# Kernel tuning notes

Hardware: AMD Instinct MI355X
Metric: run time of the kernel (lower is better)

## Reference

```python
import jax, jax.numpy as jnp
import numpy as np


def gcn_conv(x, src, dst, W, b, num_nodes):
    # PyG GCNConv: add self-loops, symmetric deg^-1/2 normalization, scatter-add.
    h = x @ W                                    # [N, out]
    loops = jnp.arange(num_nodes, dtype=src.dtype)
    s = jnp.concatenate([src, loops])            # [E+N]
    d = jnp.concatenate([dst, loops])            # [E+N]
    deg = jax.ops.segment_sum(jnp.ones_like(d, dtype=h.dtype), d, num_segments=num_nodes)
    dinv = jnp.where(deg > 0, jax.lax.rsqrt(deg), 0.0)
    norm = dinv[s] * dinv[d]                     # [E+N]
    msgs = h[s] * norm[:, None]                  # gather + scale  [E+N, out]
    out = jax.ops.segment_sum(msgs, d, num_segments=num_nodes)
    return out + b


NUM_GRAPHS = 512


def setup_inputs() -> dict:
    key = jax.random.key(0)
    ks = jax.random.split(key, 12)
    N, E, F = 50000, 400000, 128
    x = jax.random.normal(ks[0], (N, F), dtype=jnp.float32)
    edge_index = jax.random.randint(ks[1], (2, E), 0, N, dtype=jnp.int64)
    batch = jnp.sort(jax.random.randint(ks[2], (N,), 0, NUM_GRAPHS, dtype=jnp.int64))
    def lin(k, fi, fo):
        return jax.random.normal(k, (fi, fo), dtype=jnp.float32) * (1.0 / np.sqrt(fi))
    return {
        "x": x, "edge_index": edge_index, "batch": batch,
        "W1": lin(ks[3], F, 512), "b1": jnp.zeros((512,), jnp.float32),
        "W2": lin(ks[4], 512, 256), "b2": jnp.zeros((256,), jnp.float32),
        "W3": lin(ks[5], 256, 128), "b3": jnp.zeros((128,), jnp.float32),
        "W4": lin(ks[6], 128, 32), "b4": jnp.zeros((32,), jnp.float32),
        "W5": lin(ks[7], 32, 10), "b5": jnp.zeros((10,), jnp.float32),
    }


def reference(x, edge_index, batch, W1, b1, W2, b2, W3, b3, W4, b4, W5, b5):
    N = x.shape[0]
    src, dst = edge_index[0], edge_index[1]
    h = gcn_conv(x, src, dst, W1, b1, N)
    h = jax.nn.leaky_relu(h, negative_slope=0.01)
    h = gcn_conv(h, src, dst, W2, b2, N)          # [N, 256]
    embs = jax.ops.segment_max(h, batch, num_segments=NUM_GRAPHS)  # [G, 256]
    z = ((h @ W3 + b3) @ W4 + b4) @ W5 + b5       # [N, 10]
    out = jax.ops.segment_max(z, batch, num_segments=NUM_GRAPHS)   # [G, 10]
    return (out, embs)
```

## Files before the change

### kernel.cpp

```cpp
#include <hip/hip_runtime.h>
#include <math.h>

#define DIV_UP(a,b) (((a)+(b)-1)/(b))

typedef __attribute__((ext_vector_type(8))) short bf16x8;
typedef __attribute__((ext_vector_type(4))) float f32x4;

__device__ inline unsigned short f2b(float x) {
    unsigned int u = __float_as_uint(x);
    u += 0x7fffu + ((u >> 16) & 1u);
    return (unsigned short)(u >> 16);
}

__device__ inline void cvt8(uint4 v, float* a) {
    a[0] = __uint_as_float(v.x << 16); a[1] = __uint_as_float(v.x & 0xffff0000u);
    a[2] = __uint_as_float(v.y << 16); a[3] = __uint_as_float(v.y & 0xffff0000u);
    a[4] = __uint_as_float(v.z << 16); a[5] = __uint_as_float(v.z & 0xffff0000u);
    a[6] = __uint_as_float(v.w << 16); a[7] = __uint_as_float(v.w & 0xffff0000u);
}

__device__ inline void atomicMaxF(float* addr, float v) {
    if (v >= 0.f) atomicMax((int*)addr, __float_as_int(v));
    else          atomicMin((unsigned int*)addr, __float_as_uint(v));
}

__device__ inline void gl16(void* lds, const void* g) {
    __builtin_amdgcn_global_load_lds(
        (const __attribute__((address_space(1))) void*)g,
        (__attribute__((address_space(3))) void*)lds, 16, 0, 0);
}

__global__ void k_zero_i(int* p, int n) {
    int i = blockIdx.x * blockDim.x + threadIdx.x;
    if (i < n) p[i] = 0;
}

__global__ void k_hist(const int* __restrict__ dst, int* __restrict__ hist, int E) {
    int i = blockIdx.x * blockDim.x + threadIdx.x;
    if (i < E) atomicAdd(&hist[dst[i]], 1);
}

__global__ __launch_bounds__(256) void k_scan_bsum(const int* __restrict__ hist,
                                                   int* __restrict__ bsum, int N) {
    __shared__ int red[256];
    int t = threadIdx.x;
    int base = blockIdx.x * 1024 + t * 4;
    int s = 0;
    if (base + 3 < N) {
        int4 v = *(const int4*)&hist[base];
        s = v.x + v.y + v.z + v.w;
    } else {
        for (int j = 0; j < 4; ++j) if (base + j < N) s += hist[base + j];
    }
    red[t] = s;
    __syncthreads();
    for (int off = 128; off >= 1; off >>= 1) {
        if (t < off) red[t] += red[t + off];
        __syncthreads();
    }
    if (t == 0) bsum[blockIdx.x] = red[0];
}

__global__ __launch_bounds__(1024) void k_scan_boff(const int* __restrict__ bsum,
        int* __restrict__ boff, int* __restrict__ row_off, int NB, int N) {
    __shared__ int s[1024];
    int t = threadIdx.x;
    int v = (t < NB) ? bsum[t] : 0;
    s[t] = v;
    __syncthreads();
    for (int off = 1; off < 1024; off <<= 1) {
        int u = (t >= off) ? s[t - off] : 0;
        __syncthreads();
        s[t] += u;
        __syncthreads();
    }
    if (t < NB) boff[t] = s[t] - v;
    if (t == NB - 1) row_off[N] = s[t];
}

__global__ __launch_bounds__(256) void k_scan_apply(const int* __restrict__ hist,
        const int* __restrict__ boff, int* __restrict__ row_off,
        float* __restrict__ dinv, int N) {
    __shared__ int s[256];
    int t = threadIdx.x;
    int base = blockIdx.x * 1024 + t * 4;
    int v[4];
    int loc = 0;
#pragma unroll
    for (int j = 0; j < 4; ++j) { v[j] = (base + j < N) ? hist[base + j] : 0; loc += v[j]; }
    s[t] = loc;
    __syncthreads();
    for (int off = 1; off < 256; off <<= 1) {
        int u = (t >= off) ? s[t - off] : 0;
        __syncthreads();
        s[t] += u;
        __syncthreads();
    }
    int run = boff[blockIdx.x] + s[t] - loc;
#pragma unroll
    for (int j = 0; j < 4; ++j) {
        if (base + j < N) {
            row_off[base + j] = run;
            dinv[base + j] = rsqrtf((float)(v[j] + 1));
        }
        run += v[j];
    }
}

__global__ void k_bin(const int* __restrict__ src, const int* __restrict__ dst,
                      const int* __restrict__ row_off, int* __restrict__ cursor,
                      const float* __restrict__ dinv,
                      int* __restrict__ csr_src, float* __restrict__ csr_w, int E) {
    int i = blockIdx.x * blockDim.x + threadIdx.x;
    if (i >= E) return;
    int d = dst[i], s = src[i];
    int pos = row_off[d] + atomicAdd(&cursor[d], 1);
    csr_src[pos] = s;
    csr_w[pos] = dinv[s] * dinv[d];
}

__global__ __launch_bounds__(256) void k_pre(
        const float* __restrict__ W3, const float* __restrict__ W4,
        const float* __restrict__ W5, const float* __restrict__ b3,
        const float* __restrict__ b4, const float* __restrict__ b5,
        float* __restrict__ WcT, float* __restrict__ bc,
        unsigned* __restrict__ outp, int nout, int nfo,
        const float* __restrict__ x, unsigned short* __restrict__ xb, int n4,
        const float* __restrict__ W1, unsigned short* __restrict__ w1t, int K1, int N1,
        const float* __restrict__ W2, unsigned short* __restrict__ w2t, int K2, int N2) {
    int b = blockIdx.x;
    int t = threadIdx.x;
    if (b < 11) {
        int c = b;
        if (c < 10) {
            __shared__ float Tc[128];
            if (t < 128) {
                float s = 0.f;
#pragma unroll 8
                for (int k = 0; k < 32; ++k) s = fmaf(W4[t * 32 + k], W5[k * 10 + c], s);
                Tc[t] = s;
            }
            __syncthreads();
            float s = 0.f;
            const float* w3r = &W3[t * 128];
#pragma unroll 8
            for (int j = 0; j < 128; ++j) s = fmaf(w3r[j], Tc[j], s);
            WcT[c * 256 + t] = s;
        } else {
            __shared__ float v[32];
            if (t < 32) {
                float s = b4[t];
                for (int j = 0; j < 128; ++j) s = fmaf(b3[j], W4[j * 32 + t], s);
                v[t] = s;
            }
            __syncthreads();
            if (t < 10) {
                float s = b5[t];
                for (int k = 0; k < 32; ++k) s = fmaf(v[k], W5[k * 10 + t], s);
                bc[t] = s;
            }
        }
        return;
    }
    if (b < 11 + nfo) {
        int i = (b - 11) * 256 + t;
        if (i < nout) outp[i] = 0xff800000u;
        return;
    }
    int i = (b - 11 - nfo) * 256 + t;
    if (i < n4) {
        float4 v = ((const float4*)x)[i];
        ushort4 o;
        o.x = f2b(v.x); o.y = f2b(v.y); o.z = f2b(v.z); o.w = f2b(v.w);
        ((ushort4*)xb)[i] = o;
        return;
    }
    i -= n4;
    if (i < K1 * N1) {
        int k = i / N1, n = i % N1;
        w1t[(size_t)n * K1 + k] = f2b(W1[i]);
        return;
    }
    i -= K1 * N1;
    if (i < K2 * N2) {
        int k = i / N2, n = i % N2;
        w2t[(size_t)n * K2 + k] = f2b(W2[i]);
    }
}

template <int F>
__global__ __launch_bounds__(256) void k_gather_b(const unsigned short* __restrict__ H,
        const int* __restrict__ row_off, const int* __restrict__ csr_src,
        const float* __restrict__ csr_w, const float* __restrict__ dinv,
        const float* __restrict__ bias, unsigned short* __restrict__ outb, int N) {
    const int LPN = F / 8;
    const int NPB = 256 / LPN;
    int node = blockIdx.x * NPB + threadIdx.x / LPN;
    if (node >= N) return;
    int f = (threadIdx.x % LPN) * 8;
    const unsigned short* Hf = H + f;
    float sc = dinv[node]; sc *= sc;
    float a[8];
    cvt8(*(const uint4*)&Hf[(size_t)node * F], a);
#pragma unroll
    for (int j = 0; j < 8; ++j) a[j] *= sc;
    if (bias) {
#pragma unroll
        for (int j = 0; j < 8; ++j) a[j] += bias[f + j];
    }
    int e0 = row_off[node], e1 = row_off[node + 1];
    int e = e0;
    for (; e + 4 <= e1; e += 4) {
        int s0 = csr_src[e + 0], s1 = csr_src[e + 1];
        int s2 = csr_src[e + 2], s3 = csr_src[e + 3];
        uint4 v0 = *(const uint4*)&Hf[(size_t)s0 * F];
        uint4 v1 = *(const uint4*)&Hf[(size_t)s1 * F];
        uint4 v2 = *(const uint4*)&Hf[(size_t)s2 * F];
        uint4 v3 = *(const uint4*)&Hf[(size_t)s3 * F];
        float w0 = csr_w[e + 0], w1 = csr_w[e + 1];
        float w2 = csr_w[e + 2], w3 = csr_w[e + 3];
        float b0[8], b1[8], b2[8], b3[8];
        cvt8(v0, b0); cvt8(v1, b1); cvt8(v2, b2); cvt8(v3, b3);
#pragma unroll
        for (int j = 0; j < 8; ++j) {
            a[j] = fmaf(w0, b0[j], a[j]);
            a[j] = fmaf(w1, b1[j], a[j]);
            a[j] = fmaf(w2, b2[j], a[j]);
            a[j] = fmaf(w3, b3[j], a[j]);
        }
    }
    for (; e < e1; ++e) {
        int s = csr_src[e];
        float w = csr_w[e];
        float b[8];
        cvt8(*(const uint4*)&Hf[(size_t)s * F], b);
#pragma unroll
        for (int j = 0; j < 8; ++j) a[j] = fmaf(w, b[j], a[j]);
    }
    uint4 o;
    o.x = (unsigned)f2b(a[0]) | ((unsigned)f2b(a[1]) << 16);
    o.y = (unsigned)f2b(a[2]) | ((unsigned)f2b(a[3]) << 16);
    o.z = (unsigned)f2b(a[4]) | ((unsigned)f2b(a[5]) << 16);
    o.w = (unsigned)f2b(a[6]) | ((unsigned)f2b(a[7]) << 16);
    *(uint4*)&outb[(size_t)node * F + f] = o;
}

__global__ __launch_bounds__(256) void k_gather_head(
        const unsigned short* __restrict__ H,
        const int* __restrict__ row_off, const int* __restrict__ csr_src,
        const float* __restrict__ csr_w, const float* __restrict__ dinv,
        const float* __restrict__ bias, const int* __restrict__ batch,
        const float* __restrict__ WcT, const float* __restrict__ bc,
        float* __restrict__ out, float* __restrict__ out_emb, int N) {
    __shared__ __align__(16) float Ws[10][260];
    __shared__ float bs[10];
    __shared__ __align__(16) float h2s[8][264];
    __shared__ float zl[8][10];
    __shared__ int gl[8];
    int t = threadIdx.x;
    for (int i = t; i < 2560; i += 256) Ws[i >> 8][i & 255] = WcT[i];
    if (t < 10) bs[t] = bc[t];
    int nl = t >> 5;
    int q  = t & 31;
    int node = blockIdx.x * 8 + nl;
    bool valid = node < N;
    if (q == 0) gl[nl] = valid ? batch[node] : -1;
    int f = q * 8;
    const unsigned short* Hf = H + f;
    float a[8] = {0.f, 0.f, 0.f, 0.f, 0.f, 0.f, 0.f, 0.f};
    if (valid) {
        float sc = dinv[node]; sc *= sc;
        cvt8(*(const uint4*)&Hf[(size_t)node * 256], a);
#pragma unroll
        for (int j = 0; j < 8; ++j) a[j] = fmaf(a[j], sc, bias[f + j]);
        int e0 = row_off[node], e1 = row_off[node + 1];
        int e = e0;
        for (; e + 4 <= e1; e += 4) {
            int s0 = csr_src[e + 0], s1 = csr_src[e + 1];
            int s2 = csr_src[e + 2], s3 = csr_src[e + 3];
            uint4 v0 = *(const uint4*)&Hf[(size_t)s0 * 256];
            uint4 v1 = *(const uint4*)&Hf[(size_t)s1 * 256];
            uint4 v2 = *(const uint4*)&Hf[(size_t)s2 * 256];
            uint4 v3 = *(const uint4*)&Hf[(size_t)s3 * 256];
            float w0 = csr_w[e + 0], w1 = csr_w[e + 1];
            float w2 = csr_w[e + 2], w3 = csr_w[e + 3];
            float b0[8], b1[8], b2v[8], b3v[8];
            cvt8(v0, b0); cvt8(v1, b1); cvt8(v2, b2v); cvt8(v3, b3v);
#pragma unroll
            for (int j = 0; j < 8; ++j) {
                a[j] = fmaf(w0, b0[j], a[j]);
                a[j] = fmaf(w1, b1[j], a[j]);
                a[j] = fmaf(w2, b2v[j], a[j]);
                a[j] = fmaf(w3, b3v[j], a[j]);
            }
        }
        for (; e < e1; ++e) {
            int s = csr_src[e];
            float w = csr_w[e];
            float bv[8];
            cvt8(*(const uint4*)&Hf[(size_t)s * 256], bv);
#pragma unroll
            for (int j = 0; j < 8; ++j) a[j] = fmaf(w, bv[j], a[j]);
        }
    }
    __syncthreads();

#pragma unroll
    for (int c = 0; c < 10; ++c) {
        float4 wa = *(const float4*)&Ws[c][f];
        float4 wb = *(const float4*)&Ws[c][f + 4];
        float s = a[0] * wa.x;
        s = fmaf(a[1], wa.y, s);
        s = fmaf(a[2], wa.z, s);
        s = fmaf(a[3], wa.w, s);
        s = fmaf(a[4], wb.x, s);
        s = fmaf(a[5], wb.y, s);
        s = fmaf(a[6], wb.z, s);
        s = fmaf(a[7], wb.w, s);
        s += __shfl_xor(s, 16);
        s += __shfl_xor(s, 8);
        s += __shfl_xor(s, 4);
        s += __shfl_xor(s, 2);
        s += __shfl_xor(s, 1);
        if (q == 0) zl[nl][c] = s + bs[c];
    }
    *(float4*)&h2s[nl][f]     = make_float4(a[0], a[1], a[2], a[3]);
    *(float4*)&h2s[nl][f + 4] = make_float4(a[4], a[5], a[6], a[7]);
    __syncthreads();

    {
        int curg = -1; float m = 0.f;
#pragma unroll
        for (int n = 0; n < 8; ++n) {
            int g = gl[n];
            if (g < 0) continue;
            float v = h2s[n][t];
            if (g != curg) {
                if (curg >= 0) atomicMaxF(&out_emb[(size_t)curg * 256 + t], m);
                curg = g; m = v;
            } else {
                m = fmaxf(m, v);
            }
        }
        if (curg >= 0) atomicMaxF(&out_emb[(size_t)curg * 256 + t], m);
    }
    if (t < 10) {
        int curg = -1; float m = 0.f;
#pragma unroll
        for (int n = 0; n < 8; ++n) {
            int g = gl[n];
            if (g < 0) continue;
            float v = zl[n][t];
            if (g != curg) {
                if (curg >= 0) atomicMaxF(&out[(size_t)curg * 10 + t], m);
                curg = g; m = v;
            } else {
                m = fmaxf(m, v);
            }
        }
        if (curg >= 0) atomicMaxF(&out[(size_t)curg * 10 + t], m);
    }
}

template <int OUT_BF16, int ACT>
__global__ __launch_bounds__(512) void k_gemm_mfma256(const unsigned short* __restrict__ A,
        const unsigned short* __restrict__ Bt, const float* __restrict__ bias,
        void* __restrict__ Cout, int M, int K, int NC) {
    __shared__ __align__(16) unsigned short As[128][64];
    __shared__ __align__(16) unsigned short Bs[256][64];
    int tid = threadIdx.x;
    int wave = tid >> 6, lane = tid & 63;
    int row0 = blockIdx.y * 128, col0 = blockIdx.x * 256;
    int wr = (wave >> 2) * 64, wc = (wave & 3) * 64;
    f32x4 acc[4][4] = {};
    int lr = lane & 15;
    int lg = lane >> 4;
    int sw = ((lane & 7) ^ (lane >> 3)) << 3;
    int ch0 = (lg ^ (lr & 7)) << 3;
    int ch1 = ch0 ^ (4 << 3);

    for (int k0 = 0; k0 < K; k0 += 64) {
#pragma unroll
        for (int c = 0; c < 2; ++c) {
            int rl = c * 64 + wave * 8 + (lane >> 3);
            int gr = min(row0 + rl, M - 1);
            gl16(&As[c * 64 + wave * 8][0], &A[(size_t)gr * K + k0 + sw]);
        }
#pragma unroll
        for (int c = 0; c < 4; ++c) {
            int rl = c * 64 + wave * 8 + (lane >> 3);
            gl16(&Bs[c * 64 + wave * 8][0], &Bt[(size_t)(col0 + rl) * K + k0 + sw]);
        }
        __syncthreads();
        bf16x8 af[2][4], bv[2][4];
#pragma unroll
        for (int i = 0; i < 4; ++i) {
            int ra = wr + i * 16 + lr;
            int rb = wc + i * 16 + lr;
            af[0][i] = *(const bf16x8*)&As[ra][ch0];
            af[1][i] = *(const bf16x8*)&As[ra][ch1];
            bv[0][i] = *(const bf16x8*)&Bs[rb][ch0];
            bv[1][i] = *(const bf16x8*)&Bs[rb][ch1];
        }
#pragma unroll
        for (int s = 0; s < 2; ++s)
#pragma unroll
            for (int i = 0; i < 4; ++i)
#pragma unroll
                for (int j = 0; j < 4; ++j)
                    acc[i][j] = __builtin_amdgcn_mfma_f32_16x16x32_bf16(bv[s][j], af[s][i], acc[i][j], 0, 0, 0);
        __syncthreads();
    }

    int q4 = lg * 4;
    float4 bb[4];
#pragma unroll
    for (int j = 0; j < 4; ++j)
        bb[j] = bias ? *(const float4*)&bias[col0 + wc + j * 16 + q4]
                     : make_float4(0.f, 0.f, 0.f, 0.f);
#pragma unroll
    for (int i = 0; i < 4; ++i) {
        int row = row0 + wr + i * 16 + lr;
        if (row >= M) continue;
#pragma unroll
        for (int j = 0; j < 4; ++j) {
            int c0 = col0 + wc + j * 16 + q4;
            float4 v;
            v.x = acc[i][j][0] + bb[j].x;
            v.y = acc[i][j][1] + bb[j].y;
            v.z = acc[i][j][2] + bb[j].z;
            v.w = acc[i][j][3] + bb[j].w;
            if (ACT) {
                v.x = (v.x >= 0.f) ? v.x : 0.01f * v.x;
                v.y = (v.y >= 0.f) ? v.y : 0.01f * v.y;
                v.z = (v.z >= 0.f) ? v.z : 0.01f * v.z;
                v.w = (v.w >= 0.f) ? v.w : 0.01f * v.w;
            }
            if (OUT_BF16) {
                uint2 o;
                o.x = (unsigned)f2b(v.x) | ((unsigned)f2b(v.y) << 16);
                o.y = (unsigned)f2b(v.z) | ((unsigned)f2b(v.w) << 16);
                *(uint2*)&((unsigned short*)Cout)[(size_t)row * NC + c0] = o;
            } else {
                *(float4*)&((float*)Cout)[(size_t)row * NC + c0] = v;
            }
        }
    }
}

extern "C" void kernel_launch(void* const* d_in, const int* in_sizes, int n_in,
                              void* d_out, int out_size, void* d_ws, size_t ws_size,
                              hipStream_t stream) {
    const float* x  = (const float*)d_in[0];
    const int* ei   = (const int*)d_in[1];
    const int* batch= (const int*)d_in[2];
    const float* W1 = (const float*)d_in[3];
    const float* b1 = (const float*)d_in[4];
    const float* W2 = (const float*)d_in[5];
    const float* b2 = (const float*)d_in[6];
    const float* W3 = (const float*)d_in[7];
    const float* b3 = (const float*)d_in[8];
    const float* W4 = (const float*)d_in[9];
    const float* b4 = (const float*)d_in[10];
    const float* W5 = (const float*)d_in[11];
    const float* b5 = (const float*)d_in[12];

    const int N  = in_sizes[2];
    const int F  = in_sizes[0] / N;
    const int E  = in_sizes[1] / 2;
    const int C1 = in_sizes[4];
    const int C2 = in_sizes[6];
    const int C5 = in_sizes[12];
    const int G  = out_size / (C2 + C5);
    const int NB = DIV_UP(N, 1024);

    const int* srcp = ei;
    const int* dstp = ei + E;

    uintptr_t p = (uintptr_t)d_ws;
    auto carve = [&](size_t bytes) {
        uintptr_t r = p;
        p += (bytes + 255) & ~(size_t)255;
        return (void*)r;
    };
    int* hist    = (int*)carve(sizeof(int) * N);
    int* cursor  = (int*)carve(sizeof(int) * N);
    int* row_off = (int*)carve(sizeof(int) * (N + 1));
    int* bsum    = (int*)carve(sizeof(int) * NB);
    int* boff    = (int*)carve(sizeof(int) * NB);
    int* csr_src = (int*)carve(sizeof(int) * E);
    float* csr_w = (float*)carve(sizeof(float) * E);
    float* dinv  = (float*)carve(sizeof(float) * N);
    float* wct   = (float*)carve(sizeof(float) * C2 * C5);
    float* bcv   = (float*)carve(sizeof(float) * C5);
    unsigned short* w1t = (unsigned short*)carve(sizeof(short) * F * C1);
    unsigned short* w2t = (unsigned short*)carve(sizeof(short) * C1 * C2);
    unsigned short* xb    = (unsigned short*)carve(sizeof(short) * (size_t)N * F);
    unsigned short* aggxb = (unsigned short*)carve(sizeof(short) * (size_t)N * F);
    unsigned short* h1b   = (unsigned short*)carve(sizeof(short) * (size_t)N * C1);
    unsigned short* t2b   = (unsigned short*)carve(sizeof(short) * (size_t)N * C2);

    float* out     = (float*)d_out;
    float* out_emb = out + (size_t)G * C5;

    int zspan = (int)(((sizeof(int) * N + 255) & ~(size_t)255) / 4) + N;
    k_zero_i<<<DIV_UP(zspan, 256), 256, 0, stream>>>(hist, zspan);
    k_hist<<<DIV_UP(E, 256), 256, 0, stream>>>(dstp, hist, E);
    k_scan_bsum<<<NB, 256, 0, stream>>>(hist, bsum, N);
    k_scan_boff<<<1, 1024, 0, stream>>>(bsum, boff, row_off, NB, N);
    k_scan_apply<<<NB, 256, 0, stream>>>(hist, boff, row_off, dinv, N);
    k_bin<<<DIV_UP(E, 256), 256, 0, stream>>>(srcp, dstp, row_off, cursor, dinv,
                                              csr_src, csr_w, E);

    int n4 = N * F / 4;
    int nout = G * (C2 + C5);
    int nfo = DIV_UP(nout, 256);
    int prep_total = n4 + F * C1 + C1 * C2;
    int pre_blocks = 11 + nfo + DIV_UP(prep_total, 256);
    k_pre<<<pre_blocks, 256, 0, stream>>>(W3, W4, W5, b3, b4, b5, wct, bcv,
                                          (unsigned*)d_out, nout, nfo,
                                          x, xb, n4, W1, w1t, F, C1, W2, w2t, C1, C2);

    k_gather_b<128><<<DIV_UP(N, 16), 256, 0, stream>>>(
        xb, row_off, csr_src, csr_w, dinv, nullptr, aggxb, N);
    dim3 g1(C1 / 256, DIV_UP(N, 128));
    k_gemm_mfma256<1, 1><<<g1, 512, 0, stream>>>(aggxb, w1t, b1, h1b, N, F, C1);

    dim3 g2(C2 / 256, DIV_UP(N, 128));
    k_gemm_mfma256<1, 0><<<g2, 512, 0, stream>>>(h1b, w2t, nullptr, t2b, N, C1, C2);

    k_gather_head<<<DIV_UP(N, 8), 256, 0, stream>>>(
        t2b, row_off, csr_src, csr_w, dinv, b2, batch, wct, bcv,
        out, out_emb, N);
}
```

Before: 274.2 us.

## Stage edge lists in LDS and software-pipeline neighbor row gathers

Both gather kernels now have the lanes of each node cooperatively copy up to 32 edge indices and weights into shared memory. A shared helper then gathers neighbor feature rows with a double-buffered prefetch: the next four rows load while the current four are converted and accumulated. Tails are handled by padding with a clamped index and zero weight. The head kernel also stops staging the classifier weights in LDS and drops a block barrier, reading the weights from global memory instead. The aim is to hide random-gather latency, at the cost of more registers and a fallback loop for nodes with more than 32 edges.

After: 276.7 us. No clear change (+0.9%).

```diff
diff --git a/kernel.cpp b/kernel.cpp
--- a/kernel.cpp
+++ b/kernel.cpp
@@ -28,6 +28,64 @@
     __builtin_amdgcn_global_load_lds(
         (const __attribute__((address_space(1))) void*)g,
         (__attribute__((address_space(3))) void*)lds, 16, 0, 0);
+}
+
+template <int F>
+__device__ inline void edge_accum(const unsigned short* __restrict__ Hf,
+        const int* __restrict__ sIdxRow, const float* __restrict__ sWtRow,
+        int cap, float* a) {
+    if (cap <= 0) return;
+    int cm = cap - 1;
+    int k = 0;
+    int s0 = sIdxRow[0];
+    int s1 = sIdxRow[min(1, cm)];
+    int s2 = sIdxRow[min(2, cm)];
+    int s3 = sIdxRow[min(3, cm)];
+    uint4 vA0 = *(const uint4*)&Hf[(size_t)s0 * F];
+    uint4 vA1 = *(const uint4*)&Hf[(size_t)s1 * F];
+    uint4 vA2 = *(const uint4*)&Hf[(size_t)s2 * F];
+    uint4 vA3 = *(const uint4*)&Hf[(size_t)s3 * F];
+    float bb[8];
+    while (k + 4 < cap) {
+        int m1 = min(k + 5, cm), m2 = min(k + 6, cm), m3 = min(k + 7, cm);
+        int t0 = sIdxRow[k + 4], t1 = sIdxRow[m1], t2 = sIdxRow[m2], t3 = sIdxRow[m3];
+        uint4 vB0 = *(const uint4*)&Hf[(size_t)t0 * F];
+        uint4 vB1 = *(const uint4*)&Hf[(size_t)t1 * F];
+        uint4 vB2 = *(const uint4*)&Hf[(size_t)t2 * F];
+        uint4 vB3 = *(const uint4*)&Hf[(size_t)t3 * F];
+        __builtin_amdgcn_sched_barrier(0);
+        float w0 = sWtRow[k], w1 = sWtRow[k + 1], w2 = sWtRow[k + 2], w3 = sWtRow[k + 3];
+        cvt8(vA0, bb);
+#pragma unroll
+        for (int j = 0; j < 8; ++j) a[j] = fmaf(w0, bb[j], a[j]);
+        cvt8(vA1, bb);
+#pragma unroll
+        for (int j = 0; j < 8; ++j) a[j] = fmaf(w1, bb[j], a[j]);
+        cvt8(vA2, bb);
+#pragma unroll
+        for (int j = 0; j < 8; ++j) a[j] = fmaf(w2, bb[j], a[j]);
+        cvt8(vA3, bb);
+#pragma unroll
+        for (int j = 0; j < 8; ++j) a[j] = fmaf(w3, bb[j], a[j]);
+        vA0 = vB0; vA1 = vB1; vA2 = vB2; vA3 = vB3;
+        k += 4;
+    }
+    float w0 = sWtRow[k];
+    float w1 = (k + 1 <= cm) ? sWtRow[k + 1] : 0.f;
+    float w2 = (k + 2 <= cm) ? sWtRow[k + 2] : 0.f;
+    float w3 = (k + 3 <= cm) ? sWtRow[k + 3] : 0.f;
+    cvt8(vA0, bb);
+#pragma unroll
+    for (int j = 0; j < 8; ++j) a[j] = fmaf(w0, bb[j], a[j]);
+    cvt8(vA1, bb);
+#pragma unroll
+    for (int j = 0; j < 8; ++j) a[j] = fmaf(w1, bb[j], a[j]);
+    cvt8(vA2, bb);
+#pragma unroll
+    for (int j = 0; j < 8; ++j) a[j] = fmaf(w2, bb[j], a[j]);
+    cvt8(vA3, bb);
+#pragma unroll
+    for (int j = 0; j < 8; ++j) a[j] = fmaf(w3, bb[j], a[j]);
 }
 
 __global__ void k_zero_i(int* p, int n) {
@@ -188,61 +246,45 @@
     }
 }
 
-template <int F>
-__global__ __launch_bounds__(256) void k_gather_b(const unsigned short* __restrict__ H,
+__global__ __launch_bounds__(256) void k_gather1(const unsigned short* __restrict__ H,
         const int* __restrict__ row_off, const int* __restrict__ csr_src,
         const float* __restrict__ csr_w, const float* __restrict__ dinv,
-        const float* __restrict__ bias, unsigned short* __restrict__ outb, int N) {
-    const int LPN = F / 8;
-    const int NPB = 256 / LPN;
-    int node = blockIdx.x * NPB + threadIdx.x / LPN;
+        unsigned short* __restrict__ outb, int N) {
+    __shared__ int   sIdx[16][32];
+    __shared__ float sWt[16][32];
+    int t = threadIdx.x;
+    int nl = t >> 4, q = t & 15;
+    int node = blockIdx.x * 16 + nl;
     if (node >= N) return;
-    int f = (threadIdx.x % LPN) * 8;
+    int f = q * 8;
     const unsigned short* Hf = H + f;
     float sc = dinv[node]; sc *= sc;
     float a[8];
-    cvt8(*(const uint4*)&Hf[(size_t)node * F], a);
+    cvt8(*(const uint4*)&Hf[(size_t)node * 128], a);
 #pragma unroll
     for (int j = 0; j < 8; ++j) a[j] *= sc;
-    if (bias) {
-#pragma unroll
-        for (int j = 0; j < 8; ++j) a[j] += bias[f + j];
-    }
     int e0 = row_off[node], e1 = row_off[node + 1];
-    int e = e0;
-    for (; e + 4 <= e1; e += 4) {
-        int s0 = csr_src[e + 0], s1 = csr_src[e + 1];
-        int s2 = csr_src[e + 2], s3 = csr_src[e + 3];
-        uint4 v0 = *(const uint4*)&Hf[(size_t)s0 * F];
-        uint4 v1 = *(const uint4*)&Hf[(size_t)s1 * F];
-        uint4 v2 = *(const uint4*)&Hf[(size_t)s2 * F];
-        uint4 v3 = *(const uint4*)&Hf[(size_t)s3 * F];
-        float w0 = csr_w[e + 0], w1 = csr_w[e + 1];
-        float w2 = csr_w[e + 2], w3 = csr_w[e + 3];
-        float b0[8], b1[8], b2[8], b3[8];
-        cvt8(v0, b0); cvt8(v1, b1); cvt8(v2, b2); cvt8(v3, b3);
-#pragma unroll
-        for (int j = 0; j < 8; ++j) {
-            a[j] = fmaf(w0, b0[j], a[j]);
-            a[j] = fmaf(w1, b1[j], a[j]);
-            a[j] = fmaf(w2, b2[j], a[j]);
-            a[j] = fmaf(w3, b3[j], a[j]);
-        }
-    }
-    for (; e < e1; ++e) {
-        int s = csr_src[e];
-        float w = csr_w[e];
-        float b[8];
-        cvt8(*(const uint4*)&Hf[(size_t)s * F], b);
-#pragma unroll
-        for (int j = 0; j < 8; ++j) a[j] = fmaf(w, b[j], a[j]);
+    int deg = e1 - e0;
+    int cap = min(deg, 32);
+    if (q < cap)      { sIdx[nl][q]      = csr_src[e0 + q];      sWt[nl][q]      = csr_w[e0 + q]; }
+    if (q + 16 < cap) { sIdx[nl][q + 16] = csr_src[e0 + q + 16]; sWt[nl][q + 16] = csr_w[e0 + q + 16]; }
+    edge_accum<128>(Hf, &sIdx[nl][0], &sWt[nl][0], cap, a);
+    if (deg > 32) {
+        for (int e = e0 + 32; e < e1; ++e) {
+            int s = csr_src[e];
+            float w = csr_w[e];
+            float bb[8];
+            cvt8(*(const uint4*)&Hf[(size_t)s * 128], bb);
+#pragma unroll
+            for (int j = 0; j < 8; ++j) a[j] = fmaf(w, bb[j], a[j]);
+        }
     }
     uint4 o;
     o.x = (unsigned)f2b(a[0]) | ((unsigned)f2b(a[1]) << 16);
     o.y = (unsigned)f2b(a[2]) | ((unsigned)f2b(a[3]) << 16);
     o.z = (unsigned)f2b(a[4]) | ((unsigned)f2b(a[5]) << 16);
     o.w = (unsigned)f2b(a[6]) | ((unsigned)f2b(a[7]) << 16);
-    *(uint4*)&outb[(size_t)node * F + f] = o;
+    *(uint4*)&outb[(size_t)node * 128 + f] = o;
 }
 
 __global__ __launch_bounds__(256) void k_gather_head(
@@ -252,14 +294,12 @@
         const float* __restrict__ bias, const int* __restrict__ batch,
         const float* __restrict__ WcT, const float* __restrict__ bc,
         float* __restrict__ out, float* __restrict__ out_emb, int N) {
-    __shared__ __align__(16) float Ws[10][260];
-    __shared__ float bs[10];
     __shared__ __align__(16) float h2s[8][264];
     __shared__ float zl[8][10];
     __shared__ int gl[8];
+    __shared__ int   sIdx[8][32];
+    __shared__ float sWt[8][32];
     int t = threadIdx.x;
-    for (int i = t; i < 2560; i += 256) Ws[i >> 8][i & 255] = WcT[i];
-    if (t < 10) bs[t] = bc[t];
     int nl = t >> 5;
     int q  = t & 31;
     int node = blockIdx.x * 8 + nl;
@@ -274,41 +314,26 @@
 #pragma unroll
         for (int j = 0; j < 8; ++j) a[j] = fmaf(a[j], sc, bias[f + j]);
         int e0 = row_off[node], e1 = row_off[node + 1];
-        int e = e0;
-        for (; e + 4 <= e1; e += 4) {
-            int s0 = csr_src[e + 0], s1 = csr_src[e + 1];
-            int s2 = csr_src[e + 2], s3 = csr_src[e + 3];
-            uint4 v0 = *(const uint4*)&Hf[(size_t)s0 * 256];
-            uint4 v1 = *(const uint4*)&Hf[(size_t)s1 * 256];
-            uint4 v2 = *(const uint4*)&Hf[(size_t)s2 * 256];
-            uint4 v3 = *(const uint4*)&Hf[(size_t)s3 * 256];
-            float w0 = csr_w[e + 0], w1 = csr_w[e + 1];
-            float w2 = csr_w[e + 2], w3 = csr_w[e + 3];
-            float b0[8], b1[8], b2v[8], b3v[8];
-            cvt8(v0, b0); cvt8(v1, b1); cvt8(v2, b2v); cvt8(v3, b3v);
-#pragma unroll
-            for (int j = 0; j < 8; ++j) {
-                a[j] = fmaf(w0, b0[j], a[j]);
-                a[j] = fmaf(w1, b1[j], a[j]);
-                a[j] = fmaf(w2, b2v[j], a[j]);
-                a[j] = fmaf(w3, b3v[j], a[j]);
-            }
-        }
-        for (; e < e1; ++e) {
-            int s = csr_src[e];
-            float w = csr_w[e];
-            float bv[8];
-            cvt8(*(const uint4*)&Hf[(size_t)s * 256], bv);
-#pragma unroll
-            for (int j = 0; j < 8; ++j) a[j] = fmaf(w, bv[j], a[j]);
-        }
-    }
-    __syncthreads();
+        int deg = e1 - e0;
+        int cap = min(deg, 32);
+        if (q < cap) { sIdx[nl][q] = csr_src[e0 + q]; sWt[nl][q] = csr_w[e0 + q]; }
+        edge_accum<256>(Hf, &sIdx[nl][0], &sWt[nl][0], cap, a);
+        if (deg > 32) {
+            for (int e = e0 + 32; e < e1; ++e) {
+                int s = csr_src[e];
+                float w = csr_w[e];
+                float bb[8];
+                cvt8(*(const uint4*)&Hf[(size_t)s * 256], bb);
+#pragma unroll
+                for (int j = 0; j < 8; ++j) a[j] = fmaf(w, bb[j], a[j]);
+            }
+        }
+    }
 
 #pragma unroll
     for (int c = 0; c < 10; ++c) {
-        float4 wa = *(const float4*)&Ws[c][f];
-        float4 wb = *(const float4*)&Ws[c][f + 4];
+        float4 wa = *(const float4*)&WcT[c * 256 + f];
+        float4 wb = *(const float4*)&WcT[c * 256 + f + 4];
         float s = a[0] * wa.x;
         s = fmaf(a[1], wa.y, s);
         s = fmaf(a[2], wa.z, s);
@@ -322,7 +347,7 @@
         s += __shfl_xor(s, 4);
         s += __shfl_xor(s, 2);
         s += __shfl_xor(s, 1);
-        if (q == 0) zl[nl][c] = s + bs[c];
+        if (q == 0) zl[nl][c] = s + bc[c];
     }
     *(float4*)&h2s[nl][f]     = make_float4(a[0], a[1], a[2], a[3]);
     *(float4*)&h2s[nl][f + 4] = make_float4(a[4], a[5], a[6], a[7]);
@@ -521,8 +546,8 @@
                                           (unsigned*)d_out, nout, nfo,
                                           x, xb, n4, W1, w1t, F, C1, W2, w2t, C1, C2);
 
-    k_gather_b<128><<<DIV_UP(N, 16), 256, 0, stream>>>(
-        xb, row_off, csr_src, csr_w, dinv, nullptr, aggxb, N);
+    k_gather1<<<DIV_UP(N, 16), 256, 0, stream>>>(
+        xb, row_off, csr_src, csr_w, dinv, aggxb, N);
     dim3 g1(C1 / 256, DIV_UP(N, 128));
     k_gemm_mfma256<1, 1><<<g1, 512, 0, stream>>>(aggxb, w1t, b1, h1b, N, F, C1);
 
```
